# Kernel optimization log

Measured on AMD Instinct MI355X. Metric: run time of the kernel, lower is better.

The kernel has to match this reference:

```python
import jax, jax.numpy as jnp
import numpy as np

EMBED = 768
N_HEADS = 12
HEAD = EMBED // N_HEADS  # 64
B, T = 2, 2048


def setup_inputs() -> dict:
    key = jax.random.key(0)
    ks = jax.random.split(key, 5)
    s = 0.02
    return {
        "x": jax.random.normal(ks[0], (B, T, EMBED), dtype=jnp.float32),
        "w_attn": jax.random.normal(ks[1], (EMBED, 3 * EMBED), dtype=jnp.float32) * s,
        "b_attn": jnp.zeros((3 * EMBED,), dtype=jnp.float32),
        "w_proj": jax.random.normal(ks[2], (EMBED, EMBED), dtype=jnp.float32) * s,
        "b_proj": jnp.zeros((EMBED,), dtype=jnp.float32),
    }


def reference(x, w_attn, b_attn, w_proj, b_proj):
    b, t, c = x.shape
    scale = HEAD ** -0.5
    qkv = x @ w_attn + b_attn  # [b,t,3c]
    q, k, v = jnp.split(qkv, 3, axis=-1)

    # einops 'b t (h n) -> b n t h' with n=N_HEADS: channel dim factors as
    # (head_size, n_heads) — head index is the inner factor.
    def split_heads(u):
        return u.reshape(b, t, HEAD, N_HEADS).transpose(0, 3, 1, 2)  # [b,n,t,h]

    q, k, v = split_heads(q), split_heads(k), split_heads(v)

    scores = jnp.einsum("bnth,bnsh->bnts", q, k) * scale  # [b,n,t,t]
    causal = jnp.tril(jnp.ones((t, t), dtype=bool))
    scores = jnp.where(causal, scores, jnp.finfo(scores.dtype).min)
    weights = jax.nn.softmax(scores, axis=-1)
    att = jnp.einsum("bnts,bnsh->bnth", weights, v)  # [b,n,t,h]

    # 'b n t h -> b t (n h)': heads are the OUTER factor on output
    att = att.transpose(0, 2, 1, 3).reshape(b, t, c)
    return att @ w_proj + b_proj
```

## Files before the change

### kernel.cpp

```cpp
#include <hip/hip_runtime.h>
#include <hip/hip_bf16.h>
#include <math.h>

#define NB      2
#define T_SZ    2048
#define EMBEDC  768
#define NHEADS  12
#define HEADD   64
#define QKV_PER (NB * NHEADS * T_SZ * HEADD)
#define QSCALE  0.18033688011112042f

typedef __bf16 bf16x8 __attribute__((ext_vector_type(8)));
typedef float  f32x4  __attribute__((ext_vector_type(4)));
typedef float  f32x16 __attribute__((ext_vector_type(16)));

__device__ inline ushort f2bf(float x) {
    union { float f; uint u; } v; v.f = x;
    uint r = v.u + 0x7fffu + ((v.u >> 16) & 1u);
    return (ushort)(r >> 16);
}

__device__ inline uint pack2bf(float a, float b) {
    union { __bf16 h[2]; uint u; } t;
    t.h[0] = (__bf16)a; t.h[1] = (__bf16)b;
    return t.u;
}

__device__ inline void gload16(const ushort* g, ushort* l) {
    __builtin_amdgcn_global_load_lds(
        (const __attribute__((address_space(1))) unsigned int*)g,
        (__attribute__((address_space(3))) unsigned int*)l, 16, 0, 0);
}

__global__ __launch_bounds__(256) void cast_k(const float* __restrict__ in,
                                              ushort* __restrict__ out, int n)
{
    int i = (blockIdx.x * 256 + threadIdx.x) * 8;
    if (i >= n) return;
    float4 a = *(const float4*)(in + i);
    float4 b = *(const float4*)(in + i + 4);
    union { ushort u[8]; int4 v; } p;
    p.u[0] = f2bf(a.x); p.u[1] = f2bf(a.y); p.u[2] = f2bf(a.z); p.u[3] = f2bf(a.w);
    p.u[4] = f2bf(b.x); p.u[5] = f2bf(b.y); p.u[6] = f2bf(b.z); p.u[7] = f2bf(b.w);
    *(int4*)(out + i) = p.v;
}

template <int PERM>
__global__ __launch_bounds__(256) void tcast_k(const float* __restrict__ in,
                                               ushort* __restrict__ out,
                                               int R, int C)
{
    __shared__ float t[32][33];
    const int c0 = blockIdx.x * 32, r0 = blockIdx.y * 32;
    const int tx = threadIdx.x & 31, ty = threadIdx.x >> 5;
#pragma unroll
    for (int u = 0; u < 4; ++u)
        t[ty + 8 * u][tx] = in[(size_t)(r0 + ty + 8 * u) * C + c0 + tx];
    __syncthreads();
#pragma unroll
    for (int u = 0; u < 4; ++u) {
        int n = c0 + ty + 8 * u;
        int orow = n;
        if (PERM) {
            int mat = n / EMBEDC, cc = n % EMBEDC;
            orow = mat * EMBEDC + (cc % NHEADS) * HEADD + cc / NHEADS;
        }
        out[(size_t)orow * R + r0 + tx] = f2bf(t[tx][ty + 8 * u]);
    }
}

#define STAGE(buf, koff)                                        \
    do {                                                        \
        gload16(gA0 + (koff), &As[buf][lA0o]);                  \
        gload16(gA1 + (koff), &As[buf][lA1o]);                  \
        gload16(gB0 + (koff), &Bs[buf][lB0o]);                  \
        gload16(gB1 + (koff), &Bs[buf][lB1o]);                  \
    } while (0)

template <int MODE>
__global__ __launch_bounds__(256) void gemm_bf16_k(
    const ushort* __restrict__ A, const ushort* __restrict__ Bt,
    const float* __restrict__ bias, void* __restrict__ outp,
    int M, int N, int K)
{
    __shared__ ushort As[2][128 * 32];
    __shared__ ushort Bs[2][128 * 32];

    const int tid = threadIdx.x;
    const int w = tid >> 6, l = tid & 63;
    const int g = l >> 4, r16 = l & 15;
    const int wr = w >> 1, wc = w & 1;
    const int m0 = blockIdx.y * 128, n0 = blockIdx.x * 128;

    const int srow = l >> 2;
    const int scol = ((l & 3) ^ (srow & 3)) * 8;
    const ushort* gA0 = A + (size_t)(m0 + 32 * w + srow) * K + scol;
    const ushort* gA1 = gA0 + (size_t)16 * K;
    const ushort* gB0 = Bt + (size_t)(n0 + 32 * w + srow) * K + scol;
    const ushort* gB1 = gB0 + (size_t)16 * K;
    const int lA0o = (32 * w) * 32,      lA1o = (32 * w + 16) * 32;
    const int lB0o = lA0o,               lB1o = lA1o;

    f32x4 acc[4][4];
#pragma unroll
    for (int i = 0; i < 4; ++i)
#pragma unroll
        for (int j = 0; j < 4; ++j) acc[i][j] = (f32x4){0.f, 0.f, 0.f, 0.f};

    const int rck = (r16 & 3);

    STAGE(0, 0);
    __syncthreads();

    int cur = 0;
    for (int k0 = 0; k0 < K; k0 += 32) {
        if (k0 + 32 < K) STAGE(cur ^ 1, k0 + 32);

        const ushort* sA = As[cur];
        const ushort* sB = Bs[cur];
        bf16x8 af[4], bfr[4];
#pragma unroll
        for (int ms = 0; ms < 4; ++ms) {
            int row = 64 * wr + 16 * ms + r16;
            af[ms] = *(const bf16x8*)&sA[row * 32 + ((g ^ rck) * 8)];
        }
#pragma unroll
        for (int ns = 0; ns < 4; ++ns) {
            int row = 64 * wc + 16 * ns + r16;
            bfr[ns] = *(const bf16x8*)&sB[row * 32 + ((g ^ rck) * 8)];
        }
#pragma unroll
        for (int ms = 0; ms < 4; ++ms)
#pragma unroll
            for (int ns = 0; ns < 4; ++ns)
                acc[ms][ns] = __builtin_amdgcn_mfma_f32_16x16x32_bf16(
                    af[ms], bfr[ns], acc[ms][ns], 0, 0, 0);

        __syncthreads();
        cur ^= 1;
    }

#pragma unroll
    for (int ns = 0; ns < 4; ++ns) {
        const int n = n0 + 64 * wc + 16 * ns + r16;
        if (MODE == 0) {
            float* out = (float*)outp;
            const float bv = bias[n];
#pragma unroll
            for (int ms = 0; ms < 4; ++ms) {
                const int mb = m0 + 64 * wr + 16 * ms + 4 * g;
#pragma unroll
                for (int r = 0; r < 4; ++r)
                    out[(size_t)(mb + r) * N + n] = acc[ms][ns][r] + bv;
            }
        } else {
            ushort* ob = (ushort*)outp;
            const int mat  = n / EMBEDC;
            const int c    = n - mat * EMBEDC;
            const int head = c >> 6;
            const int hd   = c & 63;
            const float bv = bias[mat * EMBEDC + hd * NHEADS + head];
            if (mat == 2) {
#pragma unroll
                for (int ms = 0; ms < 4; ++ms) {
                    const int mb = m0 + 64 * wr + 16 * ms + 4 * g;
                    const int b = mb >> 11, t0 = mb & 2047;
                    const size_t bh = (size_t)(b * NHEADS + head);
                    uint2 pv;
                    pv.x = pack2bf(acc[ms][ns][0] + bv, acc[ms][ns][1] + bv);
                    pv.y = pack2bf(acc[ms][ns][2] + bv, acc[ms][ns][3] + bv);
                    *(uint2*)(ob + 2 * (size_t)QKV_PER +
                              (bh * HEADD + hd) * T_SZ + t0) = pv;
                }
            } else {
                const float qs = (mat == 0) ? QSCALE : 1.f;
#pragma unroll
                for (int ms = 0; ms < 4; ++ms) {
                    const int mb = m0 + 64 * wr + 16 * ms + 4 * g;
#pragma unroll
                    for (int r = 0; r < 4; ++r) {
                        const int m = mb + r;
                        const int b = m >> 11, t = m & 2047;
                        const size_t bh = (size_t)(b * NHEADS + head);
                        ob[(size_t)mat * QKV_PER + (bh * T_SZ + t) * HEADD + hd] =
                            f2bf((acc[ms][ns][r] + bv) * qs);
                    }
                }
            }
        }
    }
}

__global__ __launch_bounds__(256) void attn_mfma_k(
    const ushort* __restrict__ Qb, const ushort* __restrict__ Kb,
    const ushort* __restrict__ Vtb, ushort* __restrict__ Out)
{
    __shared__ float fsm[4 * 2048];
    __shared__ float Ml[128], Ll[128];

    const int bid = blockIdx.x;
    const int xcd = bid & 7, j = bid >> 3;
    const int bh = xcd * 3 + (j >> 6);
    const int iq = 63 - (j & 63);
    const int bb = bh / NHEADS, head = bh % NHEADS;
    const int tid = threadIdx.x;
    const int w = tid >> 6, l = tid & 63;
    const int q31 = l & 31, hi = l >> 5;
    const int q0 = iq * 32;
    const int nt = iq + 1;
    const int cpw = (nt + 3) >> 2;
    const int b0 = w * cpw;
    const int b1 = min(b0 + cpw, nt);

    const ushort* Qg = Qb + (size_t)bh * T_SZ * HEADD;
    const ushort* Kg = Kb + (size_t)bh * T_SZ * HEADD;
    const ushort* Vg = Vtb + (size_t)bh * HEADD * T_SZ;
    const ushort* V0 = Vg + (size_t)q31 * T_SZ + 8 * hi;
    const ushort* V1 = Vg + (size_t)(32 + q31) * T_SZ + 8 * hi;

    f32x16 o0, o1, z;
#pragma unroll
    for (int r = 0; r < 16; ++r) { o0[r] = 0.f; o1[r] = 0.f; z[r] = 0.f; }
    float mR = -1e30f, lR = 0.f;

    if (b0 < b1) {
        const ushort* qrow = Qg + (size_t)(q0 + q31) * HEADD + 8 * hi;
        const bf16x8 qf0 = *(const bf16x8*)(qrow);
        const bf16x8 qf1 = *(const bf16x8*)(qrow + 16);
        const bf16x8 qf2 = *(const bf16x8*)(qrow + 32);
        const bf16x8 qf3 = *(const bf16x8*)(qrow + 48);

        const ushort* Krow = Kg + (size_t)q31 * HEADD + 8 * hi;
        const ushort* kr0 = Krow + (size_t)(b0 * 32) * HEADD;
        bf16x8 kf0 = *(const bf16x8*)(kr0);
        bf16x8 kf1 = *(const bf16x8*)(kr0 + 16);
        bf16x8 kf2 = *(const bf16x8*)(kr0 + 32);
        bf16x8 kf3 = *(const bf16x8*)(kr0 + 48);

        for (int kt = b0; kt < b1; ++kt) {
            const int kvb = kt * 32;
            const bf16x8 va0 = *(const bf16x8*)(V0 + kvb);
            const bf16x8 va1 = *(const bf16x8*)(V0 + kvb + 16);
            const bf16x8 vb0 = *(const bf16x8*)(V1 + kvb);
            const bf16x8 vb1 = *(const bf16x8*)(V1 + kvb + 16);
            bf16x8 kn0, kn1, kn2, kn3;
            if (kt + 1 < b1) {
                const ushort* kr = Krow + (size_t)(kvb + 32) * HEADD;
                kn0 = *(const bf16x8*)(kr);
                kn1 = *(const bf16x8*)(kr + 16);
                kn2 = *(const bf16x8*)(kr + 32);
                kn3 = *(const bf16x8*)(kr + 48);
            }

            f32x16 st = z;
            st = __builtin_amdgcn_mfma_f32_32x32x16_bf16(kf0, qf0, st, 0, 0, 0);
            st = __builtin_amdgcn_mfma_f32_32x32x16_bf16(kf1, qf1, st, 0, 0, 0);
            st = __builtin_amdgcn_mfma_f32_32x32x16_bf16(kf2, qf2, st, 0, 0, 0);
            st = __builtin_amdgcn_mfma_f32_32x32x16_bf16(kf3, qf3, st, 0, 0, 0);

            if (kt == nt - 1) {
#pragma unroll
                for (int r = 0; r < 16; ++r)
                    if (((r & 3) + 8 * (r >> 2) + 4 * hi) > q31)
                        st[r] = -1e30f;
            }

            float pm = st[0];
#pragma unroll
            for (int r = 1; r < 16; ++r) pm = fmaxf(pm, st[r]);
            pm = fmaxf(pm, __shfl_xor(pm, 32));
            if (!__all(pm - mR <= 8.f)) {
                float mNew = fmaxf(mR, pm);
                float sc = exp2f(mR - mNew);
                lR *= sc;
                o0 *= sc;
                o1 *= sc;
                mR = mNew;
            }
            float rs = 0.f;
#pragma unroll
            for (int r = 0; r < 16; ++r) {
                float e = exp2f(st[r] - mR);
                st[r] = e;
                rs += e;
            }
            rs += __shfl_xor(rs, 32);
            lR += rs;

            uint w0 = pack2bf(st[0],  st[1]),  w1 = pack2bf(st[2],  st[3]);
            uint w2 = pack2bf(st[4],  st[5]),  w3 = pack2bf(st[6],  st[7]);
            uint w4 = pack2bf(st[8],  st[9]),  w5 = pack2bf(st[10], st[11]);
            uint w6 = pack2bf(st[12], st[13]), w7 = pack2bf(st[14], st[15]);

            uint e0 = (uint)__shfl_xor((int)(hi ? w0 : w2), 32);
            uint e1 = (uint)__shfl_xor((int)(hi ? w1 : w3), 32);
            uint e2 = (uint)__shfl_xor((int)(hi ? w4 : w6), 32);
            uint e3 = (uint)__shfl_xor((int)(hi ? w5 : w7), 32);

            union { uint u[4]; bf16x8 v; } p0, p1;
            p0.u[0] = hi ? e0 : w0;  p0.u[1] = hi ? e1 : w1;
            p0.u[2] = hi ? w2 : e0;  p0.u[3] = hi ? w3 : e1;
            p1.u[0] = hi ? e2 : w4;  p1.u[1] = hi ? e3 : w5;
            p1.u[2] = hi ? w6 : e2;  p1.u[3] = hi ? w7 : e3;

            o0 = __builtin_amdgcn_mfma_f32_32x32x16_bf16(va0, p0.v, o0, 0, 0, 0);
            o0 = __builtin_amdgcn_mfma_f32_32x32x16_bf16(va1, p1.v, o0, 0, 0, 0);
            o1 = __builtin_amdgcn_mfma_f32_32x32x16_bf16(vb0, p0.v, o1, 0, 0, 0);
            o1 = __builtin_amdgcn_mfma_f32_32x32x16_bf16(vb1, p1.v, o1, 0, 0, 0);

            kf0 = kn0; kf1 = kn1; kf2 = kn2; kf3 = kn3;
        }
    }

    if (hi == 0) {
        Ml[w * 32 + q31] = mR;
        Ll[w * 32 + q31] = lR;
    }
    const int key = 4 * (q31 & 15);
    float* img = &fsm[w * 2048 + q31 * 64];
#pragma unroll
    for (int c = 0; c < 4; ++c) {
        f32x4 s0 = {o0[4 * c + 0], o0[4 * c + 1], o0[4 * c + 2], o0[4 * c + 3]};
        f32x4 s1 = {o1[4 * c + 0], o1[4 * c + 1], o1[4 * c + 2], o1[4 * c + 3]};
        *(f32x4*)&img[(8 * c + 4 * hi) ^ key]        = s0;
        *(f32x4*)&img[((8 * c + 4 * hi) + 32) ^ key] = s1;
    }
    __syncthreads();

    {
        const int q  = tid >> 3;
        const int dc = tid & 7;
        const int gkey = 4 * (q & 15);
        float m0 = Ml[q], m1 = Ml[32 + q], m2 = Ml[64 + q], m3 = Ml[96 + q];
        float mt = fmaxf(fmaxf(m0, m1), fmaxf(m2, m3));
        float f0 = exp2f(m0 - mt), f1 = exp2f(m1 - mt);
        float f2 = exp2f(m2 - mt), f3 = exp2f(m3 - mt);
        float lt = Ll[q] * f0 + Ll[32 + q] * f1 + Ll[64 + q] * f2 + Ll[96 + q] * f3;
        const float inv = 1.f / lt;
        const float* row = &fsm[q * 64];
        f32x4 acc[2];
#pragma unroll
        for (int jj = 0; jj < 2; ++jj) {
            const int dsw = (dc * 8 + 4 * jj) ^ gkey;
            acc[jj] = *(const f32x4*)&row[dsw] * f0
                    + *(const f32x4*)&row[2048 + dsw] * f1
                    + *(const f32x4*)&row[4096 + dsw] * f2
                    + *(const f32x4*)&row[6144 + dsw] * f3;
        }
        uint4 pv;
        pv.x = pack2bf(acc[0][0] * inv, acc[0][1] * inv);
        pv.y = pack2bf(acc[0][2] * inv, acc[0][3] * inv);
        pv.z = pack2bf(acc[1][0] * inv, acc[1][1] * inv);
        pv.w = pack2bf(acc[1][2] * inv, acc[1][3] * inv);
        *(uint4*)(Out + ((size_t)(bb * T_SZ + q0 + q)) * EMBEDC
                  + head * HEADD + dc * 8) = pv;
    }
}

extern "C" void kernel_launch(void* const* d_in, const int* in_sizes, int n_in,
                              void* d_out, int out_size, void* d_ws, size_t ws_size,
                              hipStream_t stream)
{
    const float* x      = (const float*)d_in[0];
    const float* w_attn = (const float*)d_in[1];
    const float* b_attn = (const float*)d_in[2];
    const float* w_proj = (const float*)d_in[3];
    const float* b_proj = (const float*)d_in[4];
    float* out = (float*)d_out;

    ushort* qw   = (ushort*)d_ws;
    ushort* attb = qw + (size_t)3 * QKV_PER;
    ushort* xb   = attb + QKV_PER;
    ushort* waT  = xb + QKV_PER;
    ushort* wpT  = waT + (size_t)EMBEDC * 3 * EMBEDC;

    cast_k<<<QKV_PER / (256 * 8), 256, 0, stream>>>(x, xb, QKV_PER);
    tcast_k<1><<<dim3(3 * EMBEDC / 32, EMBEDC / 32), 256, 0, stream>>>(
        w_attn, waT, EMBEDC, 3 * EMBEDC);
    tcast_k<0><<<dim3(EMBEDC / 32, EMBEDC / 32), 256, 0, stream>>>(
        w_proj, wpT, EMBEDC, EMBEDC);

    gemm_bf16_k<1><<<dim3(2304 / 128, 4096 / 128), 256, 0, stream>>>(
        xb, waT, b_attn, qw, NB * T_SZ, 3 * EMBEDC, EMBEDC);

    attn_mfma_k<<<1536, 256, 0, stream>>>(
        qw, qw + QKV_PER, qw + 2 * (size_t)QKV_PER, attb);

    gemm_bf16_k<0><<<dim3(768 / 128, 4096 / 128), 256, 0, stream>>>(
        attb, wpT, b_proj, out, NB * T_SZ, EMBEDC, EMBEDC);
}
```

Before: 122.4 us.

## Process 64 query rows per attention block, reusing each K/V tile twice

Each attention block now handles two 32-row query sub-tiles, so every K and V fragment loaded from global memory feeds two sets of MFMAs and the grid halves from 1536 to 768 blocks. The cross-wave combine buffer in LDS now holds bf16 partial outputs instead of fp32, which keeps the doubled tile inside the shared-memory budget. The aim is less K/V traffic per unit of work and better MFMA density. In exchange, register pressure goes up from four output accumulators, there are fewer blocks to balance the causal workload, and rounding partial outputs to bf16 before the combine costs some precision.

```diff
diff --git a/kernel.cpp b/kernel.cpp
--- a/kernel.cpp
+++ b/kernel.cpp
@@ -24,6 +24,13 @@
     union { __bf16 h[2]; uint u; } t;
     t.h[0] = (__bf16)a; t.h[1] = (__bf16)b;
     return t.u;
+}
+
+__device__ inline float bflo(uint u) {
+    union { uint u; float f; } t; t.u = u << 16; return t.f;
+}
+__device__ inline float bfhi(uint u) {
+    union { uint u; float f; } t; t.u = u & 0xffff0000u; return t.f;
 }
 
 __device__ inline void gload16(const ushort* g, ushort* l) {
@@ -195,19 +202,19 @@
     const ushort* __restrict__ Qb, const ushort* __restrict__ Kb,
     const ushort* __restrict__ Vtb, ushort* __restrict__ Out)
 {
-    __shared__ float fsm[4 * 2048];
-    __shared__ float Ml[128], Ll[128];
+    __shared__ ushort imgs[4 * 64 * 64];
+    __shared__ float Ml[4 * 64], Ll[4 * 64];
 
     const int bid = blockIdx.x;
     const int xcd = bid & 7, j = bid >> 3;
-    const int bh = xcd * 3 + (j >> 6);
-    const int iq = 63 - (j & 63);
+    const int bh = xcd * 3 + (j >> 5);
+    const int qt = 31 - (j & 31);
     const int bb = bh / NHEADS, head = bh % NHEADS;
     const int tid = threadIdx.x;
     const int w = tid >> 6, l = tid & 63;
     const int q31 = l & 31, hi = l >> 5;
-    const int q0 = iq * 32;
-    const int nt = iq + 1;
+    const int q0 = qt * 64;
+    const int nt = 2 * (qt + 1);
     const int cpw = (nt + 3) >> 2;
     const int b0 = w * cpw;
     const int b1 = min(b0 + cpw, nt);
@@ -218,17 +225,24 @@
     const ushort* V0 = Vg + (size_t)q31 * T_SZ + 8 * hi;
     const ushort* V1 = Vg + (size_t)(32 + q31) * T_SZ + 8 * hi;
 
-    f32x16 o0, o1, z;
-#pragma unroll
-    for (int r = 0; r < 16; ++r) { o0[r] = 0.f; o1[r] = 0.f; z[r] = 0.f; }
-    float mR = -1e30f, lR = 0.f;
+    f32x16 oA0, oA1, oB0, oB1, z;
+#pragma unroll
+    for (int r = 0; r < 16; ++r) {
+        oA0[r] = 0.f; oA1[r] = 0.f; oB0[r] = 0.f; oB1[r] = 0.f; z[r] = 0.f;
+    }
+    float mR0 = -1e30f, lR0 = 0.f, mR1 = -1e30f, lR1 = 0.f;
 
     if (b0 < b1) {
-        const ushort* qrow = Qg + (size_t)(q0 + q31) * HEADD + 8 * hi;
-        const bf16x8 qf0 = *(const bf16x8*)(qrow);
-        const bf16x8 qf1 = *(const bf16x8*)(qrow + 16);
-        const bf16x8 qf2 = *(const bf16x8*)(qrow + 32);
-        const bf16x8 qf3 = *(const bf16x8*)(qrow + 48);
+        const ushort* qrA = Qg + (size_t)(q0 + q31) * HEADD + 8 * hi;
+        const ushort* qrB = Qg + (size_t)(q0 + 32 + q31) * HEADD + 8 * hi;
+        const bf16x8 qA0 = *(const bf16x8*)(qrA);
+        const bf16x8 qA1 = *(const bf16x8*)(qrA + 16);
+        const bf16x8 qA2 = *(const bf16x8*)(qrA + 32);
+        const bf16x8 qA3 = *(const bf16x8*)(qrA + 48);
+        const bf16x8 qB0 = *(const bf16x8*)(qrB);
+        const bf16x8 qB1 = *(const bf16x8*)(qrB + 16);
+        const bf16x8 qB2 = *(const bf16x8*)(qrB + 32);
+        const bf16x8 qB3 = *(const bf16x8*)(qrB + 48);
 
         const ushort* Krow = Kg + (size_t)q31 * HEADD + 8 * hi;
         const ushort* kr0 = Krow + (size_t)(b0 * 32) * HEADD;
@@ -252,108 +266,183 @@
                 kn3 = *(const bf16x8*)(kr + 48);
             }
 
-            f32x16 st = z;
-            st = __builtin_amdgcn_mfma_f32_32x32x16_bf16(kf0, qf0, st, 0, 0, 0);
-            st = __builtin_amdgcn_mfma_f32_32x32x16_bf16(kf1, qf1, st, 0, 0, 0);
-            st = __builtin_amdgcn_mfma_f32_32x32x16_bf16(kf2, qf2, st, 0, 0, 0);
-            st = __builtin_amdgcn_mfma_f32_32x32x16_bf16(kf3, qf3, st, 0, 0, 0);
-
-            if (kt == nt - 1) {
-#pragma unroll
-                for (int r = 0; r < 16; ++r)
-                    if (((r & 3) + 8 * (r >> 2) + 4 * hi) > q31)
-                        st[r] = -1e30f;
+            {
+                f32x16 st = z;
+                st = __builtin_amdgcn_mfma_f32_32x32x16_bf16(kf0, qA0, st, 0, 0, 0);
+                st = __builtin_amdgcn_mfma_f32_32x32x16_bf16(kf1, qA1, st, 0, 0, 0);
+                st = __builtin_amdgcn_mfma_f32_32x32x16_bf16(kf2, qA2, st, 0, 0, 0);
+                st = __builtin_amdgcn_mfma_f32_32x32x16_bf16(kf3, qA3, st, 0, 0, 0);
+
+                if (kt >= nt - 2) {
+                    const int dd = kvb - q0;
+#pragma unroll
+                    for (int r = 0; r < 16; ++r)
+                        if (dd + (r & 3) + 8 * (r >> 2) + 4 * hi > q31)
+                            st[r] = -1e30f;
+                }
+
+                float pm = st[0];
+#pragma unroll
+                for (int r = 1; r < 16; ++r) pm = fmaxf(pm, st[r]);
+                pm = fmaxf(pm, __shfl_xor(pm, 32));
+                if (!__all(pm - mR0 <= 8.f)) {
+                    float mNew = fmaxf(mR0, pm);
+                    float sc = exp2f(mR0 - mNew);
+                    lR0 *= sc; oA0 *= sc; oA1 *= sc; mR0 = mNew;
+                }
+                float rs = 0.f;
+#pragma unroll
+                for (int r = 0; r < 16; ++r) {
+                    float e = exp2f(st[r] - mR0);
+                    st[r] = e; rs += e;
+                }
+                rs += __shfl_xor(rs, 32);
+                lR0 += rs;
+
+                uint w0 = pack2bf(st[0],  st[1]),  w1 = pack2bf(st[2],  st[3]);
+                uint w2 = pack2bf(st[4],  st[5]),  w3 = pack2bf(st[6],  st[7]);
+                uint w4 = pack2bf(st[8],  st[9]),  w5 = pack2bf(st[10], st[11]);
+                uint w6 = pack2bf(st[12], st[13]), w7 = pack2bf(st[14], st[15]);
+                uint e0 = (uint)__shfl_xor((int)(hi ? w0 : w2), 32);
+                uint e1 = (uint)__shfl_xor((int)(hi ? w1 : w3), 32);
+                uint e2 = (uint)__shfl_xor((int)(hi ? w4 : w6), 32);
+                uint e3 = (uint)__shfl_xor((int)(hi ? w5 : w7), 32);
+                union { uint u[4]; bf16x8 v; } p0, p1;
+                p0.u[0] = hi ? e0 : w0;  p0.u[1] = hi ? e1 : w1;
+                p0.u[2] = hi ? w2 : e0;  p0.u[3] = hi ? w3 : e1;
+                p1.u[0] = hi ? e2 : w4;  p1.u[1] = hi ? e3 : w5;
+                p1.u[2] = hi ? w6 : e2;  p1.u[3] = hi ? w7 : e3;
+
+                oA0 = __builtin_amdgcn_mfma_f32_32x32x16_bf16(va0, p0.v, oA0, 0, 0, 0);
+                oA0 = __builtin_amdgcn_mfma_f32_32x32x16_bf16(va1, p1.v, oA0, 0, 0, 0);
+                oA1 = __builtin_amdgcn_mfma_f32_32x32x16_bf16(vb0, p0.v, oA1, 0, 0, 0);
+                oA1 = __builtin_amdgcn_mfma_f32_32x32x16_bf16(vb1, p1.v, oA1, 0, 0, 0);
             }
 
-            float pm = st[0];
-#pragma unroll
-            for (int r = 1; r < 16; ++r) pm = fmaxf(pm, st[r]);
-            pm = fmaxf(pm, __shfl_xor(pm, 32));
-            if (!__all(pm - mR <= 8.f)) {
-                float mNew = fmaxf(mR, pm);
-                float sc = exp2f(mR - mNew);
-                lR *= sc;
-                o0 *= sc;
-                o1 *= sc;
-                mR = mNew;
+            {
+                f32x16 st = z;
+                st = __builtin_amdgcn_mfma_f32_32x32x16_bf16(kf0, qB0, st, 0, 0, 0);
+                st = __builtin_amdgcn_mfma_f32_32x32x16_bf16(kf1, qB1, st, 0, 0, 0);
+                st = __builtin_amdgcn_mfma_f32_32x32x16_bf16(kf2, qB2, st, 0, 0, 0);
+                st = __builtin_amdgcn_mfma_f32_32x32x16_bf16(kf3, qB3, st, 0, 0, 0);
+
+                if (kt >= nt - 1) {
+                    const int dd = kvb - q0 - 32;
+#pragma unroll
+                    for (int r = 0; r < 16; ++r)
+                        if (dd + (r & 3) + 8 * (r >> 2) + 4 * hi > q31)
+                            st[r] = -1e30f;
+                }
+
+                float pm = st[0];
+#pragma unroll
+                for (int r = 1; r < 16; ++r) pm = fmaxf(pm, st[r]);
+                pm = fmaxf(pm, __shfl_xor(pm, 32));
+                if (!__all(pm - mR1 <= 8.f)) {
+                    float mNew = fmaxf(mR1, pm);
+                    float sc = exp2f(mR1 - mNew);
+                    lR1 *= sc; oB0 *= sc; oB1 *= sc; mR1 = mNew;
+                }
+                float rs = 0.f;
+#pragma unroll
+                for (int r = 0; r < 16; ++r) {
+                    float e = exp2f(st[r] - mR1);
+                    st[r] = e; rs += e;
+                }
+                rs += __shfl_xor(rs, 32);
+                lR1 += rs;
+
+                uint w0 = pack2bf(st[0],  st[1]),  w1 = pack2bf(st[2],  st[3]);
+                uint w2 = pack2bf(st[4],  st[5]),  w3 = pack2bf(st[6],  st[7]);
+                uint w4 = pack2bf(st[8],  st[9]),  w5 = pack2bf(st[10], st[11]);
+                uint w6 = pack2bf(st[12], st[13]), w7 = pack2bf(st[14], st[15]);
+                uint e0 = (uint)__shfl_xor((int)(hi ? w0 : w2), 32);
+                uint e1 = (uint)__shfl_xor((int)(hi ? w1 : w3), 32);
+                uint e2 = (uint)__shfl_xor((int)(hi ? w4 : w6), 32);
+                uint e3 = (uint)__shfl_xor((int)(hi ? w5 : w7), 32);
+                union { uint u[4]; bf16x8 v; } p0, p1;
+                p0.u[0] = hi ? e0 : w0;  p0.u[1] = hi ? e1 : w1;
+                p0.u[2] = hi ? w2 : e0;  p0.u[3] = hi ? w3 : e1;
+                p1.u[0] = hi ? e2 : w4;  p1.u[1] = hi ? e3 : w5;
+                p1.u[2] = hi ? w6 : e2;  p1.u[3] = hi ? w7 : e3;
+
+                oB0 = __builtin_amdgcn_mfma_f32_32x32x16_bf16(va0, p0.v, oB0, 0, 0, 0);
+                oB0 = __builtin_amdgcn_mfma_f32_32x32x16_bf16(va1, p1.v, oB0, 0, 0, 0);
+                oB1 = __builtin_amdgcn_mfma_f32_32x32x16_bf16(vb0, p0.v, oB1, 0, 0, 0);
+                oB1 = __builtin_amdgcn_mfma_f32_32x32x16_bf16(vb1, p1.v, oB1, 0, 0, 0);
             }
-            float rs = 0.f;
-#pragma unroll
-            for (int r = 0; r < 16; ++r) {
-                float e = exp2f(st[r] - mR);
-                st[r] = e;
-                rs += e;
-            }
-            rs += __shfl_xor(rs, 32);
-            lR += rs;
-
-            uint w0 = pack2bf(st[0],  st[1]),  w1 = pack2bf(st[2],  st[3]);
-            uint w2 = pack2bf(st[4],  st[5]),  w3 = pack2bf(st[6],  st[7]);
-            uint w4 = pack2bf(st[8],  st[9]),  w5 = pack2bf(st[10], st[11]);
-            uint w6 = pack2bf(st[12], st[13]), w7 = pack2bf(st[14], st[15]);
-
-            uint e0 = (uint)__shfl_xor((int)(hi ? w0 : w2), 32);
-            uint e1 = (uint)__shfl_xor((int)(hi ? w1 : w3), 32);
-            uint e2 = (uint)__shfl_xor((int)(hi ? w4 : w6), 32);
-            uint e3 = (uint)__shfl_xor((int)(hi ? w5 : w7), 32);
-
-            union { uint u[4]; bf16x8 v; } p0, p1;
-            p0.u[0] = hi ? e0 : w0;  p0.u[1] = hi ? e1 : w1;
-            p0.u[2] = hi ? w2 : e0;  p0.u[3] = hi ? w3 : e1;
-            p1.u[0] = hi ? e2 : w4;  p1.u[1] = hi ? e3 : w5;
-            p1.u[2] = hi ? w6 : e2;  p1.u[3] = hi ? w7 : e3;
-
-            o0 = __builtin_amdgcn_mfma_f32_32x32x16_bf16(va0, p0.v, o0, 0, 0, 0);
-            o0 = __builtin_amdgcn_mfma_f32_32x32x16_bf16(va1, p1.v, o0, 0, 0, 0);
-            o1 = __builtin_amdgcn_mfma_f32_32x32x16_bf16(vb0, p0.v, o1, 0, 0, 0);
-            o1 = __builtin_amdgcn_mfma_f32_32x32x16_bf16(vb1, p1.v, o1, 0, 0, 0);
 
             kf0 = kn0; kf1 = kn1; kf2 = kn2; kf3 = kn3;
         }
     }
 
     if (hi == 0) {
-        Ml[w * 32 + q31] = mR;
-        Ll[w * 32 + q31] = lR;
+        Ml[w * 64 + q31]      = mR0;  Ll[w * 64 + q31]      = lR0;
+        Ml[w * 64 + 32 + q31] = mR1;  Ll[w * 64 + 32 + q31] = lR1;
     }
     const int key = 4 * (q31 & 15);
-    float* img = &fsm[w * 2048 + q31 * 64];
-#pragma unroll
-    for (int c = 0; c < 4; ++c) {
-        f32x4 s0 = {o0[4 * c + 0], o0[4 * c + 1], o0[4 * c + 2], o0[4 * c + 3]};
-        f32x4 s1 = {o1[4 * c + 0], o1[4 * c + 1], o1[4 * c + 2], o1[4 * c + 3]};
-        *(f32x4*)&img[(8 * c + 4 * hi) ^ key]        = s0;
-        *(f32x4*)&img[((8 * c + 4 * hi) + 32) ^ key] = s1;
+    {
+        ushort* img = &imgs[(w * 64 + q31) * 64];
+#pragma unroll
+        for (int c = 0; c < 4; ++c) {
+            uint2 s0, s1;
+            s0.x = pack2bf(oA0[4 * c + 0], oA0[4 * c + 1]);
+            s0.y = pack2bf(oA0[4 * c + 2], oA0[4 * c + 3]);
+            s1.x = pack2bf(oA1[4 * c + 0], oA1[4 * c + 1]);
+            s1.y = pack2bf(oA1[4 * c + 2], oA1[4 * c + 3]);
+            *(uint2*)&img[(8 * c + 4 * hi) ^ key]        = s0;
+            *(uint2*)&img[((8 * c + 4 * hi) + 32) ^ key] = s1;
+        }
+    }
+    {
+        ushort* img = &imgs[(w * 64 + 32 + q31) * 64];
+#pragma unroll
+        for (int c = 0; c < 4; ++c) {
+            uint2 s0, s1;
+            s0.x = pack2bf(oB0[4 * c + 0], oB0[4 * c + 1]);
+            s0.y = pack2bf(oB0[4 * c + 2], oB0[4 * c + 3]);
+            s1.x = pack2bf(oB1[4 * c + 0], oB1[4 * c + 1]);
+            s1.y = pack2bf(oB1[4 * c + 2], oB1[4 * c + 3]);
+            *(uint2*)&img[(8 * c + 4 * hi) ^ key]        = s0;
+            *(uint2*)&img[((8 * c + 4 * hi) + 32) ^ key] = s1;
+        }
     }
     __syncthreads();
 
     {
-        const int q  = tid >> 3;
-        const int dc = tid & 7;
+        const int q  = tid >> 2;
+        const int dc = tid & 3;
         const int gkey = 4 * (q & 15);
-        float m0 = Ml[q], m1 = Ml[32 + q], m2 = Ml[64 + q], m3 = Ml[96 + q];
+        float m0 = Ml[q], m1 = Ml[64 + q], m2 = Ml[128 + q], m3 = Ml[192 + q];
         float mt = fmaxf(fmaxf(m0, m1), fmaxf(m2, m3));
         float f0 = exp2f(m0 - mt), f1 = exp2f(m1 - mt);
         float f2 = exp2f(m2 - mt), f3 = exp2f(m3 - mt);
-        float lt = Ll[q] * f0 + Ll[32 + q] * f1 + Ll[64 + q] * f2 + Ll[96 + q] * f3;
+        float lt = Ll[q] * f0 + Ll[64 + q] * f1 + Ll[128 + q] * f2 + Ll[192 + q] * f3;
         const float inv = 1.f / lt;
-        const float* row = &fsm[q * 64];
-        f32x4 acc[2];
-#pragma unroll
-        for (int jj = 0; jj < 2; ++jj) {
-            const int dsw = (dc * 8 + 4 * jj) ^ gkey;
-            acc[jj] = *(const f32x4*)&row[dsw] * f0
-                    + *(const f32x4*)&row[2048 + dsw] * f1
-                    + *(const f32x4*)&row[4096 + dsw] * f2
-                    + *(const f32x4*)&row[6144 + dsw] * f3;
-        }
-        uint4 pv;
-        pv.x = pack2bf(acc[0][0] * inv, acc[0][1] * inv);
-        pv.y = pack2bf(acc[0][2] * inv, acc[0][3] * inv);
-        pv.z = pack2bf(acc[1][0] * inv, acc[1][1] * inv);
-        pv.w = pack2bf(acc[1][2] * inv, acc[1][3] * inv);
-        *(uint4*)(Out + ((size_t)(bb * T_SZ + q0 + q)) * EMBEDC
-                  + head * HEADD + dc * 8) = pv;
+        ushort* orow = Out + ((size_t)(bb * T_SZ + q0 + q)) * EMBEDC
+                     + head * HEADD + dc * 16;
+#pragma unroll
+        for (int jj = 0; jj < 4; ++jj) {
+            const int dsw = (dc * 16 + 4 * jj) ^ gkey;
+            uint2 pv;
+            float a0, a1, a2, a3;
+            pv = *(const uint2*)&imgs[(0 * 64 + q) * 64 + dsw];
+            a0 = bflo(pv.x) * f0; a1 = bfhi(pv.x) * f0;
+            a2 = bflo(pv.y) * f0; a3 = bfhi(pv.y) * f0;
+            pv = *(const uint2*)&imgs[(1 * 64 + q) * 64 + dsw];
+            a0 += bflo(pv.x) * f1; a1 += bfhi(pv.x) * f1;
+            a2 += bflo(pv.y) * f1; a3 += bfhi(pv.y) * f1;
+            pv = *(const uint2*)&imgs[(2 * 64 + q) * 64 + dsw];
+            a0 += bflo(pv.x) * f2; a1 += bfhi(pv.x) * f2;
+            a2 += bflo(pv.y) * f2; a3 += bfhi(pv.y) * f2;
+            pv = *(const uint2*)&imgs[(3 * 64 + q) * 64 + dsw];
+            a0 += bflo(pv.x) * f3; a1 += bfhi(pv.x) * f3;
+            a2 += bflo(pv.y) * f3; a3 += bfhi(pv.y) * f3;
+            uint2 o;
+            o.x = pack2bf(a0 * inv, a1 * inv);
+            o.y = pack2bf(a2 * inv, a3 * inv);
+            *(uint2*)(orow + 4 * jj) = o;
+        }
     }
 }
 
@@ -383,7 +472,7 @@
     gemm_bf16_k<1><<<dim3(2304 / 128, 4096 / 128), 256, 0, stream>>>(
         xb, waT, b_attn, qw, NB * T_SZ, 3 * EMBEDC, EMBEDC);
 
-    attn_mfma_k<<<1536, 256, 0, stream>>>(
+    attn_mfma_k<<<768, 256, 0, stream>>>(
         qw, qw + QKV_PER, qw + 2 * (size_t)QKV_PER, attb);
 
     gemm_bf16_k<0><<<dim3(768 / 128, 4096 / 128), 256, 0, stream>>>(
```

New measurement: 126.9 us. +3.7%, slower.

## Share K/V tiles in LDS across four query-warps with double-buffered async loads

Applied to the files above, without the earlier changes.

Each block now covers 128 queries, one 32-row query tile per warp, and stages 64-key K and V tiles into double-buffered, XOR-swizzled shared memory with asynchronous global-to-LDS loads. All four warps read the shared tiles instead of each loading K/V from global memory. The old split-KV scheme and its cross-warp softmax merge through shared memory are gone, and each warp writes its output directly. Fewer blocks (384 instead of 1536) with uneven causal work per warp may reduce occupancy and balance.

```diff
diff --git a/kernel.cpp b/kernel.cpp
--- a/kernel.cpp
+++ b/kernel.cpp
@@ -195,166 +195,149 @@
     const ushort* __restrict__ Qb, const ushort* __restrict__ Kb,
     const ushort* __restrict__ Vtb, ushort* __restrict__ Out)
 {
-    __shared__ float fsm[4 * 2048];
-    __shared__ float Ml[128], Ll[128];
+    __shared__ ushort Ks[2][4096];
+    __shared__ ushort Vs[2][4096];
 
     const int bid = blockIdx.x;
     const int xcd = bid & 7, j = bid >> 3;
-    const int bh = xcd * 3 + (j >> 6);
-    const int iq = 63 - (j & 63);
+    const int bh  = xcd * 3 + (j >> 4);
+    const int g   = 15 - (j & 15);
     const int bb = bh / NHEADS, head = bh % NHEADS;
     const int tid = threadIdx.x;
     const int w = tid >> 6, l = tid & 63;
     const int q31 = l & 31, hi = l >> 5;
-    const int q0 = iq * 32;
-    const int nt = iq + 1;
-    const int cpw = (nt + 3) >> 2;
-    const int b0 = w * cpw;
-    const int b1 = min(b0 + cpw, nt);
+    const int Q0 = g * 128;
+    const int q0 = Q0 + 32 * w;
+    const int nt = (Q0 + 128) >> 6;
 
     const ushort* Qg = Qb + (size_t)bh * T_SZ * HEADD;
     const ushort* Kg = Kb + (size_t)bh * T_SZ * HEADD;
     const ushort* Vg = Vtb + (size_t)bh * HEADD * T_SZ;
-    const ushort* V0 = Vg + (size_t)q31 * T_SZ + 8 * hi;
-    const ushort* V1 = Vg + (size_t)(32 + q31) * T_SZ + 8 * hi;
+
+#define ASTG(buf, kvb)                                                        \
+    do {                                                                      \
+        _Pragma("unroll")                                                     \
+        for (int u = 0; u < 2; ++u) {                                         \
+            int s = tid + 256 * u;                                            \
+            int row = s >> 3, c8 = s & 7;                                     \
+            int sc = ((c8 ^ (row & 7)) * 8);                                  \
+            gload16(Kg + (size_t)((kvb) + row) * HEADD + sc, &Ks[buf][s * 8]);\
+            gload16(Vg + (size_t)row * T_SZ + (kvb) + sc, &Vs[buf][s * 8]);   \
+        }                                                                     \
+    } while (0)
+
+    const ushort* qrow = Qg + (size_t)(q0 + q31) * HEADD + 8 * hi;
+    const bf16x8 qf0 = *(const bf16x8*)(qrow);
+    const bf16x8 qf1 = *(const bf16x8*)(qrow + 16);
+    const bf16x8 qf2 = *(const bf16x8*)(qrow + 32);
+    const bf16x8 qf3 = *(const bf16x8*)(qrow + 48);
 
     f32x16 o0, o1, z;
 #pragma unroll
     for (int r = 0; r < 16; ++r) { o0[r] = 0.f; o1[r] = 0.f; z[r] = 0.f; }
     float mR = -1e30f, lR = 0.f;
 
-    if (b0 < b1) {
-        const ushort* qrow = Qg + (size_t)(q0 + q31) * HEADD + 8 * hi;
-        const bf16x8 qf0 = *(const bf16x8*)(qrow);
-        const bf16x8 qf1 = *(const bf16x8*)(qrow + 16);
-        const bf16x8 qf2 = *(const bf16x8*)(qrow + 32);
-        const bf16x8 qf3 = *(const bf16x8*)(qrow + 48);
-
-        const ushort* Krow = Kg + (size_t)q31 * HEADD + 8 * hi;
-        const ushort* kr0 = Krow + (size_t)(b0 * 32) * HEADD;
-        bf16x8 kf0 = *(const bf16x8*)(kr0);
-        bf16x8 kf1 = *(const bf16x8*)(kr0 + 16);
-        bf16x8 kf2 = *(const bf16x8*)(kr0 + 32);
-        bf16x8 kf3 = *(const bf16x8*)(kr0 + 48);
-
-        for (int kt = b0; kt < b1; ++kt) {
-            const int kvb = kt * 32;
-            const bf16x8 va0 = *(const bf16x8*)(V0 + kvb);
-            const bf16x8 va1 = *(const bf16x8*)(V0 + kvb + 16);
-            const bf16x8 vb0 = *(const bf16x8*)(V1 + kvb);
-            const bf16x8 vb1 = *(const bf16x8*)(V1 + kvb + 16);
-            bf16x8 kn0, kn1, kn2, kn3;
-            if (kt + 1 < b1) {
-                const ushort* kr = Krow + (size_t)(kvb + 32) * HEADD;
-                kn0 = *(const bf16x8*)(kr);
-                kn1 = *(const bf16x8*)(kr + 16);
-                kn2 = *(const bf16x8*)(kr + 32);
-                kn3 = *(const bf16x8*)(kr + 48);
+    const int kx = q31 & 7;
+
+    ASTG(0, 0);
+    __syncthreads();
+
+    int cur = 0;
+    for (int kt = 0; kt < nt; ++kt) {
+        if (kt + 1 < nt) ASTG(cur ^ 1, (kt + 1) * 64);
+
+        const int kvb = kt * 64;
+        const ushort* Kc = Ks[cur];
+        const ushort* Vc = Vs[cur];
+
+#pragma unroll
+        for (int h = 0; h < 2; ++h) {
+            const int khb = kvb + 32 * h;
+            if (khb <= q0 + 31) {
+                const int krow = 32 * h + q31;
+                const ushort* kp = &Kc[krow * 64];
+                bf16x8 kf0 = *(const bf16x8*)(kp + (((0 + hi) ^ kx) * 8));
+                bf16x8 kf1 = *(const bf16x8*)(kp + (((2 + hi) ^ kx) * 8));
+                bf16x8 kf2 = *(const bf16x8*)(kp + (((4 + hi) ^ kx) * 8));
+                bf16x8 kf3 = *(const bf16x8*)(kp + (((6 + hi) ^ kx) * 8));
+
+                f32x16 st = z;
+                st = __builtin_amdgcn_mfma_f32_32x32x16_bf16(kf0, qf0, st, 0, 0, 0);
+                st = __builtin_amdgcn_mfma_f32_32x32x16_bf16(kf1, qf1, st, 0, 0, 0);
+                st = __builtin_amdgcn_mfma_f32_32x32x16_bf16(kf2, qf2, st, 0, 0, 0);
+                st = __builtin_amdgcn_mfma_f32_32x32x16_bf16(kf3, qf3, st, 0, 0, 0);
+
+                if (khb == q0) {
+#pragma unroll
+                    for (int r = 0; r < 16; ++r)
+                        if (((r & 3) + 8 * (r >> 2) + 4 * hi) > q31)
+                            st[r] = -1e30f;
+                }
+
+                float pm = st[0];
+#pragma unroll
+                for (int r = 1; r < 16; ++r) pm = fmaxf(pm, st[r]);
+                pm = fmaxf(pm, __shfl_xor(pm, 32));
+                if (!__all(pm - mR <= 8.f)) {
+                    float mNew = fmaxf(mR, pm);
+                    float sc = exp2f(mR - mNew);
+                    lR *= sc; o0 *= sc; o1 *= sc; mR = mNew;
+                }
+                float rs = 0.f;
+#pragma unroll
+                for (int r = 0; r < 16; ++r) {
+                    float e = exp2f(st[r] - mR);
+                    st[r] = e; rs += e;
+                }
+                rs += __shfl_xor(rs, 32);
+                lR += rs;
+
+                uint w0 = pack2bf(st[0],  st[1]),  w1 = pack2bf(st[2],  st[3]);
+                uint w2 = pack2bf(st[4],  st[5]),  w3 = pack2bf(st[6],  st[7]);
+                uint w4 = pack2bf(st[8],  st[9]),  w5 = pack2bf(st[10], st[11]);
+                uint w6 = pack2bf(st[12], st[13]), w7 = pack2bf(st[14], st[15]);
+                uint e0 = (uint)__shfl_xor((int)(hi ? w0 : w2), 32);
+                uint e1 = (uint)__shfl_xor((int)(hi ? w1 : w3), 32);
+                uint e2 = (uint)__shfl_xor((int)(hi ? w4 : w6), 32);
+                uint e3 = (uint)__shfl_xor((int)(hi ? w5 : w7), 32);
+                union { uint u[4]; bf16x8 v; } p0, p1;
+                p0.u[0] = hi ? e0 : w0;  p0.u[1] = hi ? e1 : w1;
+                p0.u[2] = hi ? w2 : e0;  p0.u[3] = hi ? w3 : e1;
+                p1.u[0] = hi ? e2 : w4;  p1.u[1] = hi ? e3 : w5;
+                p1.u[2] = hi ? w6 : e2;  p1.u[3] = hi ? w7 : e3;
+
+                const ushort* vp0 = &Vc[q31 * 64];
+                const ushort* vp1 = &Vc[(32 + q31) * 64];
+                bf16x8 va0 = *(const bf16x8*)(vp0 + (((4 * h + hi)     ^ kx) * 8));
+                bf16x8 va1 = *(const bf16x8*)(vp0 + (((4 * h + 2 + hi) ^ kx) * 8));
+                bf16x8 vb0 = *(const bf16x8*)(vp1 + (((4 * h + hi)     ^ kx) * 8));
+                bf16x8 vb1 = *(const bf16x8*)(vp1 + (((4 * h + 2 + hi) ^ kx) * 8));
+
+                o0 = __builtin_amdgcn_mfma_f32_32x32x16_bf16(va0, p0.v, o0, 0, 0, 0);
+                o0 = __builtin_amdgcn_mfma_f32_32x32x16_bf16(va1, p1.v, o0, 0, 0, 0);
+                o1 = __builtin_amdgcn_mfma_f32_32x32x16_bf16(vb0, p0.v, o1, 0, 0, 0);
+                o1 = __builtin_amdgcn_mfma_f32_32x32x16_bf16(vb1, p1.v, o1, 0, 0, 0);
             }
-
-            f32x16 st = z;
-            st = __builtin_amdgcn_mfma_f32_32x32x16_bf16(kf0, qf0, st, 0, 0, 0);
-            st = __builtin_amdgcn_mfma_f32_32x32x16_bf16(kf1, qf1, st, 0, 0, 0);
-            st = __builtin_amdgcn_mfma_f32_32x32x16_bf16(kf2, qf2, st, 0, 0, 0);
-            st = __builtin_amdgcn_mfma_f32_32x32x16_bf16(kf3, qf3, st, 0, 0, 0);
-
-            if (kt == nt - 1) {
-#pragma unroll
-                for (int r = 0; r < 16; ++r)
-                    if (((r & 3) + 8 * (r >> 2) + 4 * hi) > q31)
-                        st[r] = -1e30f;
-            }
-
-            float pm = st[0];
-#pragma unroll
-            for (int r = 1; r < 16; ++r) pm = fmaxf(pm, st[r]);
-            pm = fmaxf(pm, __shfl_xor(pm, 32));
-            if (!__all(pm - mR <= 8.f)) {
-                float mNew = fmaxf(mR, pm);
-                float sc = exp2f(mR - mNew);
-                lR *= sc;
-                o0 *= sc;
-                o1 *= sc;
-                mR = mNew;
-            }
-            float rs = 0.f;
-#pragma unroll
-            for (int r = 0; r < 16; ++r) {
-                float e = exp2f(st[r] - mR);
-                st[r] = e;
-                rs += e;
-            }
-            rs += __shfl_xor(rs, 32);
-            lR += rs;
-
-            uint w0 = pack2bf(st[0],  st[1]),  w1 = pack2bf(st[2],  st[3]);
-            uint w2 = pack2bf(st[4],  st[5]),  w3 = pack2bf(st[6],  st[7]);
-            uint w4 = pack2bf(st[8],  st[9]),  w5 = pack2bf(st[10], st[11]);
-            uint w6 = pack2bf(st[12], st[13]), w7 = pack2bf(st[14], st[15]);
-
-            uint e0 = (uint)__shfl_xor((int)(hi ? w0 : w2), 32);
-            uint e1 = (uint)__shfl_xor((int)(hi ? w1 : w3), 32);
-            uint e2 = (uint)__shfl_xor((int)(hi ? w4 : w6), 32);
-            uint e3 = (uint)__shfl_xor((int)(hi ? w5 : w7), 32);
-
-            union { uint u[4]; bf16x8 v; } p0, p1;
-            p0.u[0] = hi ? e0 : w0;  p0.u[1] = hi ? e1 : w1;
-            p0.u[2] = hi ? w2 : e0;  p0.u[3] = hi ? w3 : e1;
-            p1.u[0] = hi ? e2 : w4;  p1.u[1] = hi ? e3 : w5;
-            p1.u[2] = hi ? w6 : e2;  p1.u[3] = hi ? w7 : e3;
-
-            o0 = __builtin_amdgcn_mfma_f32_32x32x16_bf16(va0, p0.v, o0, 0, 0, 0);
-            o0 = __builtin_amdgcn_mfma_f32_32x32x16_bf16(va1, p1.v, o0, 0, 0, 0);
-            o1 = __builtin_amdgcn_mfma_f32_32x32x16_bf16(vb0, p0.v, o1, 0, 0, 0);
-            o1 = __builtin_amdgcn_mfma_f32_32x32x16_bf16(vb1, p1.v, o1, 0, 0, 0);
-
-            kf0 = kn0; kf1 = kn1; kf2 = kn2; kf3 = kn3;
-        }
-    }
-
-    if (hi == 0) {
-        Ml[w * 32 + q31] = mR;
-        Ll[w * 32 + q31] = lR;
-    }
-    const int key = 4 * (q31 & 15);
-    float* img = &fsm[w * 2048 + q31 * 64];
+        }
+
+        __syncthreads();
+        cur ^= 1;
+    }
+
+    const float inv = 1.f / lR;
+    ushort* orow = Out + ((size_t)(bb * T_SZ + q0 + q31)) * EMBEDC
+                 + head * HEADD + 4 * hi;
 #pragma unroll
     for (int c = 0; c < 4; ++c) {
-        f32x4 s0 = {o0[4 * c + 0], o0[4 * c + 1], o0[4 * c + 2], o0[4 * c + 3]};
-        f32x4 s1 = {o1[4 * c + 0], o1[4 * c + 1], o1[4 * c + 2], o1[4 * c + 3]};
-        *(f32x4*)&img[(8 * c + 4 * hi) ^ key]        = s0;
-        *(f32x4*)&img[((8 * c + 4 * hi) + 32) ^ key] = s1;
-    }
-    __syncthreads();
-
-    {
-        const int q  = tid >> 3;
-        const int dc = tid & 7;
-        const int gkey = 4 * (q & 15);
-        float m0 = Ml[q], m1 = Ml[32 + q], m2 = Ml[64 + q], m3 = Ml[96 + q];
-        float mt = fmaxf(fmaxf(m0, m1), fmaxf(m2, m3));
-        float f0 = exp2f(m0 - mt), f1 = exp2f(m1 - mt);
-        float f2 = exp2f(m2 - mt), f3 = exp2f(m3 - mt);
-        float lt = Ll[q] * f0 + Ll[32 + q] * f1 + Ll[64 + q] * f2 + Ll[96 + q] * f3;
-        const float inv = 1.f / lt;
-        const float* row = &fsm[q * 64];
-        f32x4 acc[2];
-#pragma unroll
-        for (int jj = 0; jj < 2; ++jj) {
-            const int dsw = (dc * 8 + 4 * jj) ^ gkey;
-            acc[jj] = *(const f32x4*)&row[dsw] * f0
-                    + *(const f32x4*)&row[2048 + dsw] * f1
-                    + *(const f32x4*)&row[4096 + dsw] * f2
-                    + *(const f32x4*)&row[6144 + dsw] * f3;
-        }
-        uint4 pv;
-        pv.x = pack2bf(acc[0][0] * inv, acc[0][1] * inv);
-        pv.y = pack2bf(acc[0][2] * inv, acc[0][3] * inv);
-        pv.z = pack2bf(acc[1][0] * inv, acc[1][1] * inv);
-        pv.w = pack2bf(acc[1][2] * inv, acc[1][3] * inv);
-        *(uint4*)(Out + ((size_t)(bb * T_SZ + q0 + q)) * EMBEDC
-                  + head * HEADD + dc * 8) = pv;
-    }
+        uint2 pv0, pv1;
+        pv0.x = pack2bf(o0[4 * c + 0] * inv, o0[4 * c + 1] * inv);
+        pv0.y = pack2bf(o0[4 * c + 2] * inv, o0[4 * c + 3] * inv);
+        pv1.x = pack2bf(o1[4 * c + 0] * inv, o1[4 * c + 1] * inv);
+        pv1.y = pack2bf(o1[4 * c + 2] * inv, o1[4 * c + 3] * inv);
+        *(uint2*)(orow + 8 * c)      = pv0;
+        *(uint2*)(orow + 32 + 8 * c) = pv1;
+    }
+#undef ASTG
 }
 
 extern "C" void kernel_launch(void* const* d_in, const int* in_sizes, int n_in,
@@ -383,7 +366,7 @@
     gemm_bf16_k<1><<<dim3(2304 / 128, 4096 / 128), 256, 0, stream>>>(
         xb, waT, b_attn, qw, NB * T_SZ, 3 * EMBEDC, EMBEDC);
 
-    attn_mfma_k<<<1536, 256, 0, stream>>>(
+    attn_mfma_k<<<384, 256, 0, stream>>>(
         qw, qw + QKV_PER, qw + 2 * (size_t)QKV_PER, attb);
 
     gemm_bf16_k<0><<<dim3(768 / 128, 4096 / 128), 256, 0, stream>>>(
```

After: 148.5 us. 1.21x slower.
